# Kernel tuning notes

Hardware: AMD Instinct MI355X
Metric: run time of the kernel (lower is better)

Reference implementation:

```python
import jax, jax.numpy as jnp
import numpy as np

B, S, HID = 2, 2048, 2048
NH, NKV, D = 32, 4, 64
N_REP = NH // NKV
EPS = 1e-6
ROPE_THETA = 10000.0


def _rotate_half(x):
    h = x.shape[-1] // 2
    return jnp.concatenate([-x[..., h:], x[..., :h]], axis=-1)


def _rmsnorm(x, gamma):
    # RMSNorm over last dim (head_dim)
    return x * jax.lax.rsqrt(jnp.mean(x * x, axis=-1, keepdims=True) + EPS) * gamma


def setup_inputs() -> dict:
    key = jax.random.key(0)
    ks = jax.random.split(key, 8)
    hidden_states = jax.random.normal(ks[0], (B, S, HID), dtype=jnp.float32)
    # rotary cos/sin tables, shape [B, S, D]
    pos = jnp.arange(S, dtype=jnp.float32)
    inv_freq = 1.0 / (ROPE_THETA ** (jnp.arange(0, D, 2, dtype=jnp.float32) / D))
    freqs = pos[:, None] * inv_freq[None, :]            # [S, D/2]
    emb = jnp.concatenate([freqs, freqs], axis=-1)      # [S, D]
    cos = jnp.broadcast_to(jnp.cos(emb)[None], (B, S, D))
    sin = jnp.broadcast_to(jnp.sin(emb)[None], (B, S, D))
    sc = 0.02
    Wq = jax.random.normal(ks[1], (NH * D, HID), dtype=jnp.float32) * sc
    Wk = jax.random.normal(ks[2], (NKV * D, HID), dtype=jnp.float32) * sc
    Wv = jax.random.normal(ks[3], (NKV * D, HID), dtype=jnp.float32) * sc
    Wg = jax.random.normal(ks[4], (NH * D, HID), dtype=jnp.float32) * sc
    Wo = jax.random.normal(ks[5], (HID, NH * D), dtype=jnp.float32) * sc
    q_gamma = jnp.ones((D,), dtype=jnp.float32)
    k_gamma = jnp.ones((D,), dtype=jnp.float32)
    return dict(hidden_states=hidden_states, cos=cos, sin=sin,
                Wq=Wq, Wk=Wk, Wv=Wv, Wg=Wg, Wo=Wo,
                q_gamma=q_gamma, k_gamma=k_gamma)


def reference(hidden_states, cos, sin, Wq, Wk, Wv, Wg, Wo, q_gamma, k_gamma):
    b, s, _ = hidden_states.shape
    q = (hidden_states @ Wq.T).reshape(b, s, NH, D)
    k = (hidden_states @ Wk.T).reshape(b, s, NKV, D)
    v = (hidden_states @ Wv.T).reshape(b, s, NKV, D)
    gate = hidden_states @ Wg.T                       # [B, S, NH*D]
    # per-head RMSNorm on q/k
    q = _rmsnorm(q, q_gamma)
    k = _rmsnorm(k, k_gamma)
    # [B, H, S, D]
    q = q.transpose(0, 2, 1, 3)
    k = k.transpose(0, 2, 1, 3)
    v = v.transpose(0, 2, 1, 3)
    # RoPE (unsqueeze_dim=1)
    c = cos[:, None, :, :]
    sn = sin[:, None, :, :]
    q = q * c + _rotate_half(q) * sn
    k = k * c + _rotate_half(k) * sn
    # GQA: repeat kv heads
    kr = jnp.repeat(k, N_REP, axis=1)
    vr = jnp.repeat(v, N_REP, axis=1)
    scaling = D ** -0.5
    scores = jnp.einsum('bhqd,bhkd->bhqk', q, kr) * scaling
    w = jax.nn.softmax(scores.astype(jnp.float32), axis=-1).astype(q.dtype)
    out = jnp.einsum('bhqk,bhkd->bhqd', w, vr)
    out = out.transpose(0, 2, 1, 3).reshape(b, s, NH * D)
    out = out * jax.nn.sigmoid(gate)
    return out @ Wo.T
```

## Files before the change

### kernel.cpp

```cpp
#include <hip/hip_runtime.h>


#define LOG2E 1.44269504088896340736f

typedef __attribute__((ext_vector_type(4))) float f32x4;
typedef __attribute__((ext_vector_type(8))) short bf16x8;

__device__ __forceinline__ float bf2f(unsigned short u) {
  union { unsigned u; float f; } x; x.u = ((unsigned)u) << 16; return x.f;
}
__device__ __forceinline__ unsigned short f2bf(float f) {
  union { float f; unsigned u; } x; x.f = f;
  unsigned r = x.u + 0x7fffu + ((x.u >> 16) & 1u);
  return (unsigned short)(r >> 16);
}

__device__ __forceinline__ void async16(void* lds, const void* g) {
  __builtin_amdgcn_global_load_lds(
      (const __attribute__((address_space(1))) unsigned*)g,
      (__attribute__((address_space(3))) unsigned*)lds, 16, 0, 0);
}
__device__ __forceinline__ void lds_fence() {
  __asm__ volatile("s_waitcnt lgkmcnt(0)" ::: "memory");
}

__global__ __launch_bounds__(256) void cvt_f32_bf16(
    const float* __restrict__ src, unsigned short* __restrict__ dst, int n4) {
  int i = blockIdx.x * 256 + threadIdx.x;
  if (i >= n4) return;
  float4 v = reinterpret_cast<const float4*>(src)[i];
  ushort4 u;
  u.x = f2bf(v.x); u.y = f2bf(v.y); u.z = f2bf(v.z); u.w = f2bf(v.w);
  reinterpret_cast<ushort4*>(dst)[i] = u;
}

template <typename CT>
__device__ __forceinline__ void gemm128(
    const unsigned short* __restrict__ A, const unsigned short* __restrict__ W,
    CT* __restrict__ C, int m0, int n0, int ldc, int K,
    unsigned short* As, unsigned short* Bs) {
  const int tid = threadIdx.x;
  const int w = tid >> 6, l = tid & 63, quad = l >> 4, l16 = l & 15;
  const int wm = (w & 1) * 64, wn = (w >> 1) * 64;

  f32x4 acc[4][4];
  const f32x4 Z4 = {0.f, 0.f, 0.f, 0.f};
#pragma unroll
  for (int i = 0; i < 4; i++)
#pragma unroll
    for (int j = 0; j < 4; j++) acc[i][j] = Z4;

  const int srow = tid >> 2;
  const int scol = (tid & 3) * 8;
  const unsigned short* gA = A + (size_t)(m0 + srow) * K + scol;
  const unsigned short* gB = W + (size_t)(n0 + srow) * K + scol;
  unsigned short* lA = As + tid * 8;
  unsigned short* lB = Bs + tid * 8;

  for (int kb = 0; kb < K; kb += 32) {
    async16(lA,        gA + kb);
    async16(lA + 2048, gA + (size_t)64 * K + kb);
    async16(lB,        gB + kb);
    async16(lB + 2048, gB + (size_t)64 * K + kb);
    __syncthreads();

    bf16x8 af[4], bf[4];
#pragma unroll
    for (int mt = 0; mt < 4; mt++)
      af[mt] = *(const bf16x8*)&As[(wm + mt * 16 + l16) * 32 + quad * 8];
#pragma unroll
    for (int nt = 0; nt < 4; nt++)
      bf[nt] = *(const bf16x8*)&Bs[(wn + nt * 16 + l16) * 32 + quad * 8];
#pragma unroll
    for (int mt = 0; mt < 4; mt++)
#pragma unroll
      for (int nt = 0; nt < 4; nt++)
        acc[mt][nt] = __builtin_amdgcn_mfma_f32_16x16x32_bf16(
            af[mt], bf[nt], acc[mt][nt], 0, 0, 0);
    __syncthreads();
  }

#pragma unroll
  for (int mt = 0; mt < 4; mt++)
#pragma unroll
    for (int nt = 0; nt < 4; nt++) {
      int row = m0 + wm + mt * 16 + quad * 4;
      int col = n0 + wn + nt * 16 + l16;
#pragma unroll
      for (int r = 0; r < 4; r++) {
        if constexpr (sizeof(CT) == 2)
          C[(size_t)(row + r) * ldc + col] = f2bf(acc[mt][nt][r]);
        else
          C[(size_t)(row + r) * ldc + col] = acc[mt][nt][r];
      }
    }
}

__global__ __launch_bounds__(256) void gemm_qkvg(
    const unsigned short* __restrict__ X,
    const unsigned short* __restrict__ Wq, const unsigned short* __restrict__ Wk,
    const unsigned short* __restrict__ Wv, const unsigned short* __restrict__ Wg,
    unsigned short* __restrict__ Qr, unsigned short* __restrict__ Kr,
    unsigned short* __restrict__ Vr, unsigned short* __restrict__ Gr) {
  __shared__ __attribute__((aligned(16))) unsigned short As[128 * 32];
  __shared__ __attribute__((aligned(16))) unsigned short Bs[128 * 32];
  int ny = blockIdx.y;
  const unsigned short* W; unsigned short* C; int n0, ldc;
  if (ny < 16)      { W = Wq; C = Qr; n0 = ny * 128;        ldc = 2048; }
  else if (ny < 18) { W = Wk; C = Kr; n0 = (ny - 16) * 128; ldc = 256;  }
  else if (ny < 20) { W = Wv; C = Vr; n0 = (ny - 18) * 128; ldc = 256;  }
  else              { W = Wg; C = Gr; n0 = (ny - 20) * 128; ldc = 2048; }
  gemm128<unsigned short>(X, W, C, blockIdx.x * 128, n0, ldc, 2048, As, Bs);
}

__global__ __launch_bounds__(256) void gemm_out_k(
    const unsigned short* __restrict__ A, const unsigned short* __restrict__ W,
    float* __restrict__ C) {
  __shared__ __attribute__((aligned(16))) unsigned short As[128 * 32];
  __shared__ __attribute__((aligned(16))) unsigned short Bs[128 * 32];
  gemm128<float>(A, W, C, blockIdx.x * 128, blockIdx.y * 128, 2048, 2048, As, Bs);
}

__global__ __launch_bounds__(256) void prep_qkv(
    const unsigned short* __restrict__ Qr, const unsigned short* __restrict__ Kr,
    const unsigned short* __restrict__ Vr,
    const float* __restrict__ cosb, const float* __restrict__ sinb,
    const float* __restrict__ qg, const float* __restrict__ kg,
    unsigned short* __restrict__ Qn, unsigned short* __restrict__ Kn,
    unsigned short* __restrict__ Vt) {
  int idx = blockIdx.x * 4 + (threadIdx.x >> 6);
  int d = threadIdx.x & 63;
  int token = idx / 40;
  int unit = idx - token * 40;
  int b = token >> 11, s = token & 2047;

  if (unit >= 36) {
    int kvh = unit - 36;
    Vt[((size_t)(b * 4 + kvh) * 64 + d) * 2048 + s] =
        Vr[(size_t)token * 256 + kvh * 64 + d];
    return;
  }
  const unsigned short* src; const float* gamma; float scale; unsigned short* dst;
  if (unit < 32) {
    src = Qr + (size_t)token * 2048 + unit * 64;
    gamma = qg; scale = 0.125f;
    dst = Qn + ((size_t)(b * 32 + unit) * 2048 + s) * 64;
  } else {
    int kvh = unit - 32;
    src = Kr + (size_t)token * 256 + kvh * 64;
    gamma = kg; scale = 1.0f;
    dst = Kn + ((size_t)(b * 4 + kvh) * 2048 + s) * 64;
  }
  float x = bf2f(src[d]);
  float ss = x * x;
#pragma unroll
  for (int off = 32; off >= 1; off >>= 1) ss += __shfl_xor(ss, off);
  float rr = rsqrtf(ss * (1.0f / 64.0f) + 1e-6f);
  float xn = x * rr * gamma[d];
  float other = __shfl_xor(xn, 32);
  float rot = (d < 32) ? -other : other;
  size_t cs = (size_t)(b * 2048 + s) * 64 + d;
  dst[d] = f2bf((xn * cosb[cs] + rot * sinb[cs]) * scale);
}

__global__ __launch_bounds__(256, 3) void attn(
    const unsigned short* __restrict__ Qn, const unsigned short* __restrict__ Kn,
    const unsigned short* __restrict__ Vt, const unsigned short* __restrict__ gate,
    unsigned short* __restrict__ act) {
  __shared__ __attribute__((aligned(16))) unsigned short smem[24576];
  unsigned short* Ks  = smem;
  unsigned short* Vts = smem + 8192;
  unsigned short* Ps  = smem + 16384;

  const int tid = threadIdx.x, w = tid >> 6, l = tid & 63;
  const int quad = l >> 4, l16 = l & 15, l7 = l16 & 7;
  const int bh = blockIdx.y, b = bh >> 5, h = bh & 31, kvh = h >> 3;
  const int q0 = blockIdx.x * 128;

  const unsigned short* Qg = Qn + ((size_t)(b * 32 + h) * 2048 + q0) * 64;
  const unsigned short* Kg = Kn + (size_t)(b * 4 + kvh) * 2048 * 64;
  const unsigned short* Vg = Vt + (size_t)(b * 4 + kvh) * 64 * 2048;
  unsigned short* Pw = Ps + w * 2048;

  const int kq_src = ((tid & 7) ^ ((tid >> 3) & 7)) * 8;
  const int v_src  = (((tid & 15) ^ (tid >> 4)) & 15) * 8;

#pragma unroll
  for (int i = 0; i < 4; i++)
    async16(Ks + i * 2048 + tid * 8,
            Qg + (size_t)(i * 32 + (tid >> 3)) * 64 + kq_src);
  __syncthreads();
  bf16x8 qf[2][2];
#pragma unroll
  for (int mt = 0; mt < 2; mt++)
#pragma unroll
    for (int ks = 0; ks < 2; ks++) {
      int row = w * 32 + mt * 16 + l16;
      qf[mt][ks] = *(const bf16x8*)&Ks[row * 64 + ((ks * 4 + quad) ^ l7) * 8];
    }
  __syncthreads();

  const f32x4 Z4 = {0.f, 0.f, 0.f, 0.f};
  f32x4 O[2][4];
  float lp[2][4];
#pragma unroll
  for (int mt = 0; mt < 2; mt++) {
#pragma unroll
    for (int nt = 0; nt < 4; nt++) O[mt][nt] = Z4;
#pragma unroll
    for (int r = 0; r < 4; r++) lp[mt][r] = 0.f;
  }

  for (int kt = 0; kt < 16; kt++) {
    const int s0 = kt * 128;
#pragma unroll
    for (int i = 0; i < 4; i++)
      async16(Ks + i * 2048 + tid * 8,
              Kg + (size_t)(s0 + i * 32 + (tid >> 3)) * 64 + kq_src);
#pragma unroll
    for (int i = 0; i < 4; i++)
      async16(Vts + i * 2048 + tid * 8,
              Vg + (size_t)(i * 16 + (tid >> 4)) * 2048 + s0 + v_src);
    __syncthreads();

#pragma unroll
    for (int half = 0; half < 2; half++) {
      f32x4 sc[2][4];
#pragma unroll
      for (int mt = 0; mt < 2; mt++)
#pragma unroll
        for (int nt = 0; nt < 4; nt++) sc[mt][nt] = Z4;
#pragma unroll
      for (int nt = 0; nt < 4; nt++) {
        int row = half * 64 + nt * 16 + l16;
        bf16x8 kf0 = *(const bf16x8*)&Ks[row * 64 + (quad ^ l7) * 8];
        bf16x8 kf1 = *(const bf16x8*)&Ks[row * 64 + ((4 + quad) ^ l7) * 8];
#pragma unroll
        for (int mt = 0; mt < 2; mt++) {
          sc[mt][nt] = __builtin_amdgcn_mfma_f32_16x16x32_bf16(qf[mt][0], kf0, sc[mt][nt], 0, 0, 0);
          sc[mt][nt] = __builtin_amdgcn_mfma_f32_16x16x32_bf16(qf[mt][1], kf1, sc[mt][nt], 0, 0, 0);
        }
      }

#pragma unroll
      for (int mt = 0; mt < 2; mt++)
#pragma unroll
        for (int nt = 0; nt < 4; nt++)
#pragma unroll
          for (int r = 0; r < 4; r++) {
            float p = __builtin_amdgcn_exp2f(sc[mt][nt][r] * LOG2E);
            union { float f; unsigned u; } x; x.f = p;
            union { unsigned u; float f; } t; t.u = x.u & 0xffff0000u;
            lp[mt][r] += t.f;
            int q = mt * 16 + quad * 4 + r;
            int chunk = nt * 2 + (l16 >> 3);
            Pw[q * 64 + (chunk ^ (q & 7)) * 8 + l7] = (unsigned short)(x.u >> 16);
          }
      lds_fence();

#pragma unroll
      for (int ks2 = 0; ks2 < 2; ks2++) {
        bf16x8 pf[2];
#pragma unroll
        for (int mt = 0; mt < 2; mt++) {
          int q = mt * 16 + l16;
          pf[mt] = *(const bf16x8*)&Pw[q * 64 + (((ks2 * 4 + quad) ^ l7)) * 8];
        }
#pragma unroll
        for (int nt2 = 0; nt2 < 4; nt2++) {
          int vrow = nt2 * 16 + l16;
          int vchunk = half * 8 + ks2 * 4 + quad;
          bf16x8 vf = *(const bf16x8*)&Vts[vrow * 128 + (vchunk ^ l16) * 8];
#pragma unroll
          for (int mt = 0; mt < 2; mt++)
            O[mt][nt2] = __builtin_amdgcn_mfma_f32_16x16x32_bf16(
                pf[mt], vf, O[mt][nt2], 0, 0, 0);
        }
      }
      lds_fence();
    }
    __syncthreads();
  }

#pragma unroll
  for (int mt = 0; mt < 2; mt++)
#pragma unroll
    for (int r = 0; r < 4; r++) {
      float s = lp[mt][r];
#pragma unroll
      for (int off = 1; off < 16; off <<= 1) s += __shfl_xor(s, off);
      lp[mt][r] = s;
    }

#pragma unroll
  for (int mt = 0; mt < 2; mt++) {
    float inv[4];
#pragma unroll
    for (int r = 0; r < 4; r++) inv[r] = 1.0f / lp[mt][r];
#pragma unroll
    for (int nt = 0; nt < 4; nt++)
#pragma unroll
      for (int r = 0; r < 4; r++) {
        int srow = q0 + w * 32 + mt * 16 + quad * 4 + r;
        int col = h * 64 + nt * 16 + l16;
        size_t off = (size_t)(b * 2048 + srow) * 2048 + col;
        float g = bf2f(gate[off]);
        float sig = 1.0f / (1.0f + __builtin_amdgcn_exp2f(-g * LOG2E));
        act[off] = f2bf(O[mt][nt][r] * inv[r] * sig);
      }
  }
}

extern "C" void kernel_launch(void* const* d_in, const int* in_sizes, int n_in,
                              void* d_out, int out_size, void* d_ws, size_t ws_size,
                              hipStream_t stream) {
  const float* hid  = (const float*)d_in[0];
  const float* cosb = (const float*)d_in[1];
  const float* sinb = (const float*)d_in[2];
  const float* Wq   = (const float*)d_in[3];
  const float* Wk   = (const float*)d_in[4];
  const float* Wv   = (const float*)d_in[5];
  const float* Wg   = (const float*)d_in[6];
  const float* Wo   = (const float*)d_in[7];
  const float* qg   = (const float*)d_in[8];
  const float* kg   = (const float*)d_in[9];
  float* out = (float*)d_out;

  char* ws = (char*)d_ws;
  unsigned short* Xb   = (unsigned short*)(ws);
  unsigned short* WqB  = (unsigned short*)(ws + 16777216);
  unsigned short* WkB  = (unsigned short*)(ws + 25165824);
  unsigned short* WvB  = (unsigned short*)(ws + 26214400);
  unsigned short* WgB  = (unsigned short*)(ws + 27262976);
  unsigned short* WoB  = (unsigned short*)(ws + 35651584);
  unsigned short* Qraw = (unsigned short*)(ws + 44040192);
  unsigned short* Kraw = (unsigned short*)(ws + 60817408);
  unsigned short* Vraw = (unsigned short*)(ws + 62914560);
  unsigned short* gate = (unsigned short*)(ws + 65011712);
  unsigned short* Kn   = (unsigned short*)(ws + 81788928);
  unsigned short* Vt   = (unsigned short*)(ws + 83886080);
  unsigned short* Qn  = Xb;
  unsigned short* act = WqB;

  {
    struct { const float* s; unsigned short* d; int n; } jobs[6] = {
      {hid, Xb, 8388608}, {Wq, WqB, 4194304}, {Wk, WkB, 524288},
      {Wv, WvB, 524288}, {Wg, WgB, 4194304}, {Wo, WoB, 4194304}};
    for (int i = 0; i < 6; i++) {
      int n4 = jobs[i].n / 4;
      cvt_f32_bf16<<<dim3((n4 + 255) / 256), dim3(256), 0, stream>>>(
          jobs[i].s, jobs[i].d, n4);
    }
  }

  gemm_qkvg<<<dim3(32, 36), dim3(256), 0, stream>>>(
      Xb, WqB, WkB, WvB, WgB, Qraw, Kraw, Vraw, gate);

  prep_qkv<<<dim3(40960), dim3(256), 0, stream>>>(
      Qraw, Kraw, Vraw, cosb, sinb, qg, kg, Qn, Kn, Vt);

  attn<<<dim3(16, 64), dim3(256), 0, stream>>>(Qn, Kn, Vt, gate, act);

  gemm_out_k<<<dim3(32, 16), dim3(256), 0, stream>>>(act, WoB, out);
}
```

Before: 430.1 us.

## Double-buffer attention K/V tiles, fold log2e into K, merge conversion launches

Measured after the change: 411.3 us. 1.05x faster.

```diff
diff --git a/kernel.cpp b/kernel.cpp
--- a/kernel.cpp
+++ b/kernel.cpp
@@ -24,14 +24,26 @@
   __asm__ volatile("s_waitcnt lgkmcnt(0)" ::: "memory");
 }
 
-__global__ __launch_bounds__(256) void cvt_f32_bf16(
-    const float* __restrict__ src, unsigned short* __restrict__ dst, int n4) {
-  int i = blockIdx.x * 256 + threadIdx.x;
-  if (i >= n4) return;
-  float4 v = reinterpret_cast<const float4*>(src)[i];
+__global__ __launch_bounds__(256) void cvt_all(
+    const float* __restrict__ s0, const float* __restrict__ s1,
+    const float* __restrict__ s2, const float* __restrict__ s3,
+    const float* __restrict__ s4, const float* __restrict__ s5,
+    unsigned short* __restrict__ d0, unsigned short* __restrict__ d1,
+    unsigned short* __restrict__ d2, unsigned short* __restrict__ d3,
+    unsigned short* __restrict__ d4, unsigned short* __restrict__ d5) {
+  long i = (long)blockIdx.x * 256 + threadIdx.x;
+  const float* s; unsigned short* d; long off;
+  if      (i < 2097152) { s = s0; d = d0; off = 0; }
+  else if (i < 3145728) { s = s1; d = d1; off = 2097152; }
+  else if (i < 3276800) { s = s2; d = d2; off = 3145728; }
+  else if (i < 3407872) { s = s3; d = d3; off = 3276800; }
+  else if (i < 4456448) { s = s4; d = d4; off = 3407872; }
+  else                  { s = s5; d = d5; off = 4456448; }
+  long j = i - off;
+  float4 v = reinterpret_cast<const float4*>(s)[j];
   ushort4 u;
   u.x = f2bf(v.x); u.y = f2bf(v.y); u.z = f2bf(v.z); u.w = f2bf(v.w);
-  reinterpret_cast<ushort4*>(dst)[i] = u;
+  reinterpret_cast<ushort4*>(d)[j] = u;
 }
 
 template <typename CT>
@@ -148,7 +160,7 @@
   } else {
     int kvh = unit - 32;
     src = Kr + (size_t)token * 256 + kvh * 64;
-    gamma = kg; scale = 1.0f;
+    gamma = kg; scale = LOG2E;
     dst = Kn + ((size_t)(b * 4 + kvh) * 2048 + s) * 64;
   }
   float x = bf2f(src[d]);
@@ -163,14 +175,12 @@
   dst[d] = f2bf((xn * cosb[cs] + rot * sinb[cs]) * scale);
 }
 
-__global__ __launch_bounds__(256, 3) void attn(
+__global__ __launch_bounds__(256, 4) void attn(
     const unsigned short* __restrict__ Qn, const unsigned short* __restrict__ Kn,
     const unsigned short* __restrict__ Vt, const unsigned short* __restrict__ gate,
     unsigned short* __restrict__ act) {
-  __shared__ __attribute__((aligned(16))) unsigned short smem[24576];
-  unsigned short* Ks  = smem;
-  unsigned short* Vts = smem + 8192;
-  unsigned short* Ps  = smem + 16384;
+  __shared__ __attribute__((aligned(16))) unsigned short smem[20480];
+  unsigned short* Ps = smem + 16384;
 
   const int tid = threadIdx.x, w = tid >> 6, l = tid & 63;
   const int quad = l >> 4, l16 = l & 15, l7 = l16 & 7;
@@ -180,14 +190,13 @@
   const unsigned short* Qg = Qn + ((size_t)(b * 32 + h) * 2048 + q0) * 64;
   const unsigned short* Kg = Kn + (size_t)(b * 4 + kvh) * 2048 * 64;
   const unsigned short* Vg = Vt + (size_t)(b * 4 + kvh) * 64 * 2048;
-  unsigned short* Pw = Ps + w * 2048;
+  unsigned short* Pw = Ps + w * 1024;
 
   const int kq_src = ((tid & 7) ^ ((tid >> 3) & 7)) * 8;
-  const int v_src  = (((tid & 15) ^ (tid >> 4)) & 15) * 8;
 
 #pragma unroll
   for (int i = 0; i < 4; i++)
-    async16(Ks + i * 2048 + tid * 8,
+    async16(smem + i * 2048 + tid * 8,
             Qg + (size_t)(i * 32 + (tid >> 3)) * 64 + kq_src);
   __syncthreads();
   bf16x8 qf[2][2];
@@ -196,7 +205,7 @@
 #pragma unroll
     for (int ks = 0; ks < 2; ks++) {
       int row = w * 32 + mt * 16 + l16;
-      qf[mt][ks] = *(const bf16x8*)&Ks[row * 64 + ((ks * 4 + quad) ^ l7) * 8];
+      qf[mt][ks] = *(const bf16x8*)&smem[row * 64 + ((ks * 4 + quad) ^ l7) * 8];
     }
   __syncthreads();
 
@@ -211,75 +220,88 @@
     for (int r = 0; r < 4; r++) lp[mt][r] = 0.f;
   }
 
-  for (int kt = 0; kt < 16; kt++) {
-    const int s0 = kt * 128;
-#pragma unroll
-    for (int i = 0; i < 4; i++)
-      async16(Ks + i * 2048 + tid * 8,
-              Kg + (size_t)(s0 + i * 32 + (tid >> 3)) * 64 + kq_src);
-#pragma unroll
-    for (int i = 0; i < 4; i++)
-      async16(Vts + i * 2048 + tid * 8,
-              Vg + (size_t)(i * 16 + (tid >> 4)) * 2048 + s0 + v_src);
+#pragma unroll
+  for (int i = 0; i < 2; i++) {
+    async16(smem + i * 2048 + tid * 8,
+            Kg + (size_t)(i * 32 + (tid >> 3)) * 64 + kq_src);
+    async16(smem + 4096 + i * 2048 + tid * 8,
+            Vg + (size_t)(i * 32 + (tid >> 3)) * 2048 + kq_src);
+  }
+
+  for (int kt = 0; kt < 32; kt++) {
     __syncthreads();
 
-#pragma unroll
-    for (int half = 0; half < 2; half++) {
-      f32x4 sc[2][4];
+    if (kt < 31) {
+      unsigned short* nb = smem + ((kt + 1) & 1) * 8192;
+      const int s1 = (kt + 1) * 64;
+#pragma unroll
+      for (int i = 0; i < 2; i++) {
+        async16(nb + i * 2048 + tid * 8,
+                Kg + (size_t)(s1 + i * 32 + (tid >> 3)) * 64 + kq_src);
+        async16(nb + 4096 + i * 2048 + tid * 8,
+                Vg + (size_t)(i * 32 + (tid >> 3)) * 2048 + s1 + kq_src);
+      }
+    }
+
+    unsigned short* Ks  = smem + (kt & 1) * 8192;
+    unsigned short* Vts = Ks + 4096;
+
+    f32x4 sc[2][4];
+#pragma unroll
+    for (int mt = 0; mt < 2; mt++)
+#pragma unroll
+      for (int nt = 0; nt < 4; nt++) sc[mt][nt] = Z4;
+#pragma unroll
+    for (int nt = 0; nt < 4; nt++) {
+      int row = nt * 16 + l16;
+      bf16x8 kf0 = *(const bf16x8*)&Ks[row * 64 + (quad ^ l7) * 8];
+      bf16x8 kf1 = *(const bf16x8*)&Ks[row * 64 + ((4 + quad) ^ l7) * 8];
+#pragma unroll
+      for (int mt = 0; mt < 2; mt++) {
+        sc[mt][nt] = __builtin_amdgcn_mfma_f32_16x16x32_bf16(qf[mt][0], kf0, sc[mt][nt], 0, 0, 0);
+        sc[mt][nt] = __builtin_amdgcn_mfma_f32_16x16x32_bf16(qf[mt][1], kf1, sc[mt][nt], 0, 0, 0);
+      }
+    }
+
+#pragma unroll
+    for (int ks2 = 0; ks2 < 2; ks2++) {
 #pragma unroll
       for (int mt = 0; mt < 2; mt++)
 #pragma unroll
-        for (int nt = 0; nt < 4; nt++) sc[mt][nt] = Z4;
-#pragma unroll
-      for (int nt = 0; nt < 4; nt++) {
-        int row = half * 64 + nt * 16 + l16;
-        bf16x8 kf0 = *(const bf16x8*)&Ks[row * 64 + (quad ^ l7) * 8];
-        bf16x8 kf1 = *(const bf16x8*)&Ks[row * 64 + ((4 + quad) ^ l7) * 8];
-#pragma unroll
-        for (int mt = 0; mt < 2; mt++) {
-          sc[mt][nt] = __builtin_amdgcn_mfma_f32_16x16x32_bf16(qf[mt][0], kf0, sc[mt][nt], 0, 0, 0);
-          sc[mt][nt] = __builtin_amdgcn_mfma_f32_16x16x32_bf16(qf[mt][1], kf1, sc[mt][nt], 0, 0, 0);
-        }
-      }
-
-#pragma unroll
-      for (int mt = 0; mt < 2; mt++)
-#pragma unroll
-        for (int nt = 0; nt < 4; nt++)
+        for (int ntl = 0; ntl < 2; ntl++) {
+          int nt = ks2 * 2 + ntl;
 #pragma unroll
           for (int r = 0; r < 4; r++) {
-            float p = __builtin_amdgcn_exp2f(sc[mt][nt][r] * LOG2E);
+            float p = __builtin_amdgcn_exp2f(sc[mt][nt][r]);
             union { float f; unsigned u; } x; x.f = p;
             union { unsigned u; float f; } t; t.u = x.u & 0xffff0000u;
             lp[mt][r] += t.f;
             int q = mt * 16 + quad * 4 + r;
-            int chunk = nt * 2 + (l16 >> 3);
-            Pw[q * 64 + (chunk ^ (q & 7)) * 8 + l7] = (unsigned short)(x.u >> 16);
+            int c = ntl * 2 + (l16 >> 3);
+            int phys = c ^ ((q >> 1) & 3);
+            Pw[q * 32 + phys * 8 + l7] = (unsigned short)(x.u >> 16);
           }
+        }
       lds_fence();
 
-#pragma unroll
-      for (int ks2 = 0; ks2 < 2; ks2++) {
-        bf16x8 pf[2];
-#pragma unroll
-        for (int mt = 0; mt < 2; mt++) {
-          int q = mt * 16 + l16;
-          pf[mt] = *(const bf16x8*)&Pw[q * 64 + (((ks2 * 4 + quad) ^ l7)) * 8];
-        }
-#pragma unroll
-        for (int nt2 = 0; nt2 < 4; nt2++) {
-          int vrow = nt2 * 16 + l16;
-          int vchunk = half * 8 + ks2 * 4 + quad;
-          bf16x8 vf = *(const bf16x8*)&Vts[vrow * 128 + (vchunk ^ l16) * 8];
-#pragma unroll
-          for (int mt = 0; mt < 2; mt++)
-            O[mt][nt2] = __builtin_amdgcn_mfma_f32_16x16x32_bf16(
-                pf[mt], vf, O[mt][nt2], 0, 0, 0);
-        }
+      bf16x8 pf[2];
+#pragma unroll
+      for (int mt = 0; mt < 2; mt++) {
+        int q = mt * 16 + l16;
+        int phys = quad ^ ((l16 >> 1) & 3);
+        pf[mt] = *(const bf16x8*)&Pw[q * 32 + phys * 8];
+      }
+#pragma unroll
+      for (int nt2 = 0; nt2 < 4; nt2++) {
+        int d = nt2 * 16 + l16;
+        bf16x8 vf = *(const bf16x8*)&Vts[d * 64 + ((ks2 * 4 + quad) ^ l7) * 8];
+#pragma unroll
+        for (int mt = 0; mt < 2; mt++)
+          O[mt][nt2] = __builtin_amdgcn_mfma_f32_16x16x32_bf16(
+              pf[mt], vf, O[mt][nt2], 0, 0, 0);
       }
       lds_fence();
     }
-    __syncthreads();
   }
 
 #pragma unroll
@@ -342,16 +364,8 @@
   unsigned short* Qn  = Xb;
   unsigned short* act = WqB;
 
-  {
-    struct { const float* s; unsigned short* d; int n; } jobs[6] = {
-      {hid, Xb, 8388608}, {Wq, WqB, 4194304}, {Wk, WkB, 524288},
-      {Wv, WvB, 524288}, {Wg, WgB, 4194304}, {Wo, WoB, 4194304}};
-    for (int i = 0; i < 6; i++) {
-      int n4 = jobs[i].n / 4;
-      cvt_f32_bf16<<<dim3((n4 + 255) / 256), dim3(256), 0, stream>>>(
-          jobs[i].s, jobs[i].d, n4);
-    }
-  }
+  cvt_all<<<dim3(21504), dim3(256), 0, stream>>>(
+      hid, Wq, Wk, Wv, Wg, Wo, Xb, WqB, WkB, WvB, WgB, WoB);
 
   gemm_qkvg<<<dim3(32, 36), dim3(256), 0, stream>>>(
       Xb, WqB, WkB, WvB, WgB, Qraw, Kraw, Vraw, gate);
```
